# Kernel tuning notes

Hardware: AMD Instinct MI355X
Metric: run time of the kernel (lower is better)

Reference implementation:

```python
import jax, jax.numpy as jnp
import numpy as np

B, S, D, H = 2, 2048, 1024, 16
DK = D // H

def setup_inputs() -> dict:
    key = jax.random.key(0)
    ks = jax.random.split(key, 11)
    scale = 1.0 / np.sqrt(D)
    inp = {
        'query': jax.random.normal(ks[0], (B, S, D), jnp.float32),
        'key':   jax.random.normal(ks[1], (B, S, D), jnp.float32),
        'value': jax.random.normal(ks[2], (B, S, D), jnp.float32),
        'wq': jax.random.normal(ks[3], (D, D), jnp.float32) * scale,
        'bq': jax.random.normal(ks[4], (D,), jnp.float32) * 0.01,
        'wk': jax.random.normal(ks[5], (D, D), jnp.float32) * scale,
        'bk': jax.random.normal(ks[6], (D,), jnp.float32) * 0.01,
        'wv': jax.random.normal(ks[7], (D, D), jnp.float32) * scale,
        'bv': jax.random.normal(ks[8], (D,), jnp.float32) * 0.01,
        'wo': jax.random.normal(ks[9], (D, D), jnp.float32) * scale,
        'bo': jax.random.normal(ks[10], (D,), jnp.float32) * 0.01,
    }
    return inp

def reference(query, key, value, wq, bq, wk, bk, wv, bv, wo, bo):
    nb = query.shape[0]
    # projections: torch nn.Linear computes x @ W^T + b; here weights stored as (in,out)
    def proj(x, w, b):
        return (x @ w + b).reshape(nb, -1, H, DK).transpose(0, 2, 1, 3)  # [B,H,S,dk]
    q = proj(query, wq, bq)
    k = proj(key, wk, bk)
    v = proj(value, wv, bv)
    scores = jnp.einsum('bhqd,bhkd->bhqk', q, k) / jnp.sqrt(jnp.float32(DK))
    p = jax.nn.softmax(scores, axis=-1)  # dropout p=0 (eval)
    x = jnp.einsum('bhqk,bhkd->bhqd', p, v)
    x = x.transpose(0, 2, 1, 3).reshape(nb, -1, H * DK)
    return x @ wo + bo
```

## Files before the change

kernel.cpp:

```cpp
#include <hip/hip_runtime.h>


typedef __attribute__((ext_vector_type(8))) __bf16 bf16x8;
typedef __attribute__((ext_vector_type(4))) __bf16 bf16x4;
typedef __attribute__((ext_vector_type(8))) float f32x8;
typedef __attribute__((ext_vector_type(4))) float f32x4;

#define MFMA16 __builtin_amdgcn_mfma_f32_16x16x32_bf16

union Bf8 { bf16x8 v; __bf16 e[8]; };

__device__ inline f32x4 zero4() { f32x4 z; z[0]=z[1]=z[2]=z[3]=0.f; return z; }

__global__ __launch_bounds__(256) void prep_w(
        const float* __restrict__ w0, const float* __restrict__ w1,
        const float* __restrict__ w2, const float* __restrict__ w3,
        __bf16* __restrict__ wt) {
    const float* src = blockIdx.z == 0 ? w0 : blockIdx.z == 1 ? w1 :
                       blockIdx.z == 2 ? w2 : w3;
    __bf16* dst = wt + (size_t)blockIdx.z * 1048576;
    __shared__ float tile[32][33];
    const int t = threadIdx.x;
    const int tc = t & 31, tr = t >> 5;
    const int r0 = blockIdx.y * 32, c0 = blockIdx.x * 32;
#pragma unroll
    for (int i = 0; i < 4; i++) {
        int r = tr + i * 8;
        tile[r][tc] = src[(size_t)(r0 + r) * 1024 + c0 + tc];
    }
    __syncthreads();
#pragma unroll
    for (int i = 0; i < 4; i++) {
        int r = tr + i * 8;
        dst[(size_t)(c0 + r) * 1024 + r0 + tc] = (__bf16)tile[tc][r];
    }
}

__global__ __launch_bounds__(256) void prep_x(
        const float* __restrict__ x0, const float* __restrict__ x1,
        const float* __restrict__ x2, __bf16* __restrict__ xb) {
    const float* src = blockIdx.y == 0 ? x0 : blockIdx.y == 1 ? x1 : x2;
    __bf16* dst = xb + (size_t)blockIdx.y * 4194304;
    size_t g = ((size_t)blockIdx.x * 256 + threadIdx.x) * 8;
    f32x8 a = *(const f32x8*)&src[g];
    Bf8 tmp;
#pragma unroll
    for (int j = 0; j < 8; j++) tmp.e[j] = (__bf16)a[j];
    *(bf16x8*)&dst[g] = tmp.v;
}

template <int MODE, bool AF32, typename OutT>
__device__ inline void gemm_core(const void* __restrict__ Av,
                                 const __bf16* __restrict__ Bt,
                                 const float* __restrict__ bias,
                                 OutT* __restrict__ out) {
    __shared__ __bf16 As[128 * 72];
    __shared__ __bf16 Bs[128 * 72];
    const int t = threadIdx.x;
    const int wave = t >> 6, lane = t & 63, lm = lane & 15, quad = lane >> 4;
    const int m0 = blockIdx.y * 128, n0 = blockIdx.x * 128;
    const int wm = (wave >> 1) * 64, wn = (wave & 1) * 64;

    f32x4 acc[4][4];
#pragma unroll
    for (int i = 0; i < 4; i++)
#pragma unroll
        for (int j = 0; j < 4; j++) acc[i][j] = zero4();

    for (int k0 = 0; k0 < 1024; k0 += 64) {
#pragma unroll
        for (int i = 0; i < 4; i++) {
            int c = i * 256 + t;
            int row = c >> 3, c8 = c & 7;
            size_t aoff = (size_t)(m0 + row) * 1024 + k0 + c8 * 8;
            if (AF32) {
                f32x8 a = *(const f32x8*)&((const float*)Av)[aoff];
                Bf8 tmp;
#pragma unroll
                for (int j = 0; j < 8; j++) tmp.e[j] = (__bf16)a[j];
                *(bf16x8*)&As[row * 72 + c8 * 8] = tmp.v;
            } else {
                *(bf16x8*)&As[row * 72 + c8 * 8] =
                    *(const bf16x8*)&((const __bf16*)Av)[aoff];
            }
            *(bf16x8*)&Bs[row * 72 + c8 * 8] =
                *(const bf16x8*)&Bt[(size_t)(n0 + row) * 1024 + k0 + c8 * 8];
        }
        __syncthreads();
#pragma unroll
        for (int ks = 0; ks < 2; ks++) {
            bf16x8 af[4], bfr[4];
#pragma unroll
            for (int mt = 0; mt < 4; mt++)
                af[mt] = *(const bf16x8*)&As[(wm + mt * 16 + lm) * 72 + ks * 32 + quad * 8];
#pragma unroll
            for (int nt = 0; nt < 4; nt++)
                bfr[nt] = *(const bf16x8*)&Bs[(wn + nt * 16 + lm) * 72 + ks * 32 + quad * 8];
#pragma unroll
            for (int mt = 0; mt < 4; mt++)
#pragma unroll
                for (int nt = 0; nt < 4; nt++)
                    acc[mt][nt] = MFMA16(af[mt], bfr[nt], acc[mt][nt], 0, 0, 0);
        }
        __syncthreads();
    }

    float bv4[4];
#pragma unroll
    for (int nt = 0; nt < 4; nt++) bv4[nt] = bias[n0 + wn + nt * 16 + lm];

#pragma unroll
    for (int mt = 0; mt < 4; mt++) {
#pragma unroll
        for (int r = 0; r < 4; r++) {
            int row = m0 + wm + mt * 16 + quad * 4 + r;
#pragma unroll
            for (int nt = 0; nt < 4; nt++) {
                int col = n0 + wn + nt * 16 + lm;
                float val = acc[mt][nt][r] + bv4[nt];
                size_t idx;
                if (MODE == 0) {
                    idx = (size_t)row * 1024 + col;
                } else {
                    int b = row >> 11, s = row & 2047, hh = col >> 6, dk = col & 63;
                    if (MODE == 1)
                        idx = (size_t)(b * 16 + hh) * 131072 + (size_t)s * 64 + dk;
                    else
                        idx = (size_t)(b * 16 + hh) * 131072 + (size_t)dk * 2048 + s;
                }
                out[idx] = (OutT)val;
            }
        }
    }
}

template <bool AF32>
__global__ __launch_bounds__(256) void proj_kernel(
        const void* __restrict__ q, const void* __restrict__ k,
        const void* __restrict__ v, const __bf16* __restrict__ WT,
        const float* __restrict__ bq, const float* __restrict__ bk,
        const float* __restrict__ bv,
        __bf16* __restrict__ Q, __bf16* __restrict__ K, __bf16* __restrict__ Vt) {
    int z = blockIdx.z;
    if (z == 0)      gemm_core<1, AF32, __bf16>(q, WT,           bq, Q);
    else if (z == 1) gemm_core<1, AF32, __bf16>(k, WT + 1048576, bk, K);
    else             gemm_core<2, AF32, __bf16>(v, WT + 2097152, bv, Vt);
}

__global__ __launch_bounds__(256) void out_proj_kernel(
        const __bf16* __restrict__ A, const __bf16* __restrict__ Bt,
        const float* __restrict__ bias, float* __restrict__ out) {
    gemm_core<0, false, float>(A, Bt, bias, out);
}

__global__ __launch_bounds__(256, 2) void attn_kernel(
        const __bf16* __restrict__ Q, const __bf16* __restrict__ K,
        const __bf16* __restrict__ Vt, __bf16* __restrict__ O) {
    __shared__ __bf16 Ks[128 * 72];
    __shared__ __bf16 Vs[64 * 136];
    __shared__ __bf16 Ps[4 * 32 * 136];
    const int t = threadIdx.x;
    const int wave = t >> 6, lane = t & 63, lm = lane & 15, quad = lane >> 4;
    const int q0 = blockIdx.x * 128;
    const int bh = blockIdx.y;
    const size_t base = (size_t)bh * 131072;

    bf16x8 bq[2][2];
    {
        int qrow = q0 + wave * 32;
#pragma unroll
        for (int nt = 0; nt < 2; nt++)
#pragma unroll
            for (int ks = 0; ks < 2; ks++)
                bq[nt][ks] = *(const bf16x8*)
                    &Q[base + (size_t)(qrow + nt * 16 + lm) * 64 + ks * 32 + quad * 8];
    }

    float m_run[2], l_run[2];
#pragma unroll
    for (int n = 0; n < 2; n++) { m_run[n] = -1e30f; l_run[n] = 0.f; }
    f32x4 o_acc[4][2];
#pragma unroll
    for (int mt = 0; mt < 4; mt++)
#pragma unroll
        for (int n = 0; n < 2; n++) o_acc[mt][n] = zero4();

    __bf16* Pw = &Ps[wave * 32 * 136];

    for (int kv0 = 0; kv0 < 2048; kv0 += 128) {
#pragma unroll
        for (int i = 0; i < 4; i++) {
            int c = i * 256 + t;
            {
                int row = c >> 3, c8 = c & 7;
                *(bf16x8*)&Ks[row * 72 + c8 * 8] =
                    *(const bf16x8*)&K[base + (size_t)(kv0 + row) * 64 + c8 * 8];
            }
            {
                int row = c >> 4, c16 = c & 15;
                *(bf16x8*)&Vs[row * 136 + c16 * 8] =
                    *(const bf16x8*)&Vt[base + (size_t)row * 2048 + kv0 + c16 * 8];
            }
        }
        __syncthreads();

        f32x4 sc[8][2];
#pragma unroll
        for (int mt = 0; mt < 8; mt++) {
            sc[mt][0] = zero4();
            sc[mt][1] = zero4();
#pragma unroll
            for (int ks = 0; ks < 2; ks++) {
                bf16x8 ak = *(const bf16x8*)&Ks[(mt * 16 + lm) * 72 + ks * 32 + quad * 8];
                sc[mt][0] = MFMA16(ak, bq[0][ks], sc[mt][0], 0, 0, 0);
                sc[mt][1] = MFMA16(ak, bq[1][ks], sc[mt][1], 0, 0, 0);
            }
        }

#pragma unroll
        for (int nt = 0; nt < 2; nt++) {
            float mx = -1e30f;
#pragma unroll
            for (int mt = 0; mt < 8; mt++)
#pragma unroll
                for (int r = 0; r < 4; r++) {
                    sc[mt][nt][r] *= 0.125f;
                    mx = fmaxf(mx, sc[mt][nt][r]);
                }
            mx = fmaxf(mx, __shfl_xor(mx, 16));
            mx = fmaxf(mx, __shfl_xor(mx, 32));
            float mn = fmaxf(m_run[nt], mx);
            float alpha = __expf(m_run[nt] - mn);
            m_run[nt] = mn;
            float su = 0.f;
#pragma unroll
            for (int mt = 0; mt < 8; mt++)
#pragma unroll
                for (int r = 0; r < 4; r++) {
                    float p = __expf(sc[mt][nt][r] - mn);
                    sc[mt][nt][r] = p;
                    su += p;
                }
            su += __shfl_xor(su, 16);
            su += __shfl_xor(su, 32);
            l_run[nt] = l_run[nt] * alpha + su;
#pragma unroll
            for (int mt = 0; mt < 4; mt++)
#pragma unroll
                for (int r = 0; r < 4; r++) o_acc[mt][nt][r] *= alpha;
        }

#pragma unroll
        for (int nt = 0; nt < 2; nt++)
#pragma unroll
            for (int mt = 0; mt < 8; mt++) {
                bf16x4 pk;
#pragma unroll
                for (int r = 0; r < 4; r++) pk[r] = (__bf16)sc[mt][nt][r];
                *(bf16x4*)&Pw[(nt * 16 + lm) * 136 + mt * 16 + quad * 4] = pk;
            }
        __asm__ volatile("" ::: "memory");

#pragma unroll
        for (int ks = 0; ks < 4; ks++) {
            bf16x8 bp[2];
#pragma unroll
            for (int nt = 0; nt < 2; nt++)
                bp[nt] = *(const bf16x8*)&Pw[(nt * 16 + lm) * 136 + ks * 32 + quad * 8];
#pragma unroll
            for (int mt = 0; mt < 4; mt++) {
                bf16x8 av = *(const bf16x8*)&Vs[(mt * 16 + lm) * 136 + ks * 32 + quad * 8];
                o_acc[mt][0] = MFMA16(av, bp[0], o_acc[mt][0], 0, 0, 0);
                o_acc[mt][1] = MFMA16(av, bp[1], o_acc[mt][1], 0, 0, 0);
            }
        }
        __syncthreads();
    }

#pragma unroll
    for (int nt = 0; nt < 2; nt++) {
        float inv = 1.f / l_run[nt];
#pragma unroll
        for (int mt = 0; mt < 4; mt++) {
            bf16x4 pk;
#pragma unroll
            for (int r = 0; r < 4; r++) pk[r] = (__bf16)(o_acc[mt][nt][r] * inv);
            *(bf16x4*)&Pw[(nt * 16 + lm) * 136 + mt * 16 + quad * 4] = pk;
        }
    }
    __asm__ volatile("" ::: "memory");
    {
        const int b = bh >> 4, h = bh & 15;
        int ql = lane >> 1, half = lane & 1;
        int srow = q0 + wave * 32 + ql;
#pragma unroll
        for (int j = 0; j < 4; j++) {
            bf16x8 v = *(const bf16x8*)&Pw[ql * 136 + half * 32 + j * 8];
            *(bf16x8*)&O[(size_t)(b * 2048 + srow) * 1024 + h * 64 + half * 32 + j * 8] = v;
        }
    }
}

extern "C" void kernel_launch(void* const* d_in, const int* in_sizes, int n_in,
                              void* d_out, int out_size, void* d_ws, size_t ws_size,
                              hipStream_t stream) {
    if (ws_size < ((size_t)40 << 20)) return;

    const float* query = (const float*)d_in[0];
    const float* key_  = (const float*)d_in[1];
    const float* value = (const float*)d_in[2];
    const float* wq = (const float*)d_in[3];
    const float* bq = (const float*)d_in[4];
    const float* wk = (const float*)d_in[5];
    const float* bk = (const float*)d_in[6];
    const float* wv = (const float*)d_in[7];
    const float* bv = (const float*)d_in[8];
    const float* wo = (const float*)d_in[9];
    const float* bo = (const float*)d_in[10];
    float* out = (float*)d_out;

    char* ws = (char*)d_ws;
    const bool big = ws_size >= ((size_t)72 << 20);
    __bf16* WT  = (__bf16*)(ws);
    __bf16* Xb  = (__bf16*)(ws + ((size_t)8 << 20));
    size_t o0 = big ? ((size_t)32 << 20) : ((size_t)8 << 20);
    __bf16* Qw  = (__bf16*)(ws + o0);
    __bf16* Kw  = (__bf16*)(ws + o0 + ((size_t)8 << 20));
    __bf16* Vtw = (__bf16*)(ws + o0 + ((size_t)16 << 20));
    __bf16* Ow  = (__bf16*)(ws + o0 + ((size_t)24 << 20));

    prep_w<<<dim3(32, 32, 4), dim3(256), 0, stream>>>(wq, wk, wv, wo, WT);
    if (big) {
        prep_x<<<dim3(2048, 3), dim3(256), 0, stream>>>(query, key_, value, Xb);
        proj_kernel<false><<<dim3(8, 32, 3), dim3(256), 0, stream>>>(
            Xb, Xb + 4194304, Xb + 8388608, WT, bq, bk, bv, Qw, Kw, Vtw);
    } else {
        proj_kernel<true><<<dim3(8, 32, 3), dim3(256), 0, stream>>>(
            query, key_, value, WT, bq, bk, bv, Qw, Kw, Vtw);
    }
    attn_kernel<<<dim3(16, 32), dim3(256), 0, stream>>>(Qw, Kw, Vtw, Ow);
    out_proj_kernel<<<dim3(8, 32), dim3(256), 0, stream>>>(
        Ow, WT + 3 * 1048576, bo, out);
}
```

Measured before the change: 255.0 us.

## Use direct global-to-LDS loads with XOR swizzle, fuse prep kernels, fold softmax scale

Global-to-shared tile staging in the projection GEMMs and the attention K/V loads now uses the async global_load_lds builtin with an XOR-swizzled, unpadded LDS layout in place of register round-trips into padded arrays. The weight and activation conversion kernels are merged into one launch. The 1/sqrt(dk) scale moves into the Q projection epilogue so the attention loop no longer multiplies every score. Workspace layout is reshuffled so the bf16 input buffer is reused for the attention output, which lowers the threshold for the fast path. The risk is that the swizzle indexing must exactly match the per-wave LDS destination ordering of the builtin.

```diff
diff --git a/kernel.cpp b/kernel.cpp
--- a/kernel.cpp
+++ b/kernel.cpp
@@ -12,50 +12,60 @@
 
 __device__ inline f32x4 zero4() { f32x4 z; z[0]=z[1]=z[2]=z[3]=0.f; return z; }
 
-__global__ __launch_bounds__(256) void prep_w(
+__device__ inline void load_lds16(const void* g, void* l) {
+    __builtin_amdgcn_global_load_lds(
+        (const __attribute__((address_space(1))) unsigned int*)g,
+        (__attribute__((address_space(3))) unsigned int*)l, 16, 0, 0);
+}
+
+__global__ __launch_bounds__(256) void prep_all(
         const float* __restrict__ w0, const float* __restrict__ w1,
         const float* __restrict__ w2, const float* __restrict__ w3,
-        __bf16* __restrict__ wt) {
-    const float* src = blockIdx.z == 0 ? w0 : blockIdx.z == 1 ? w1 :
-                       blockIdx.z == 2 ? w2 : w3;
-    __bf16* dst = wt + (size_t)blockIdx.z * 1048576;
-    __shared__ float tile[32][33];
+        const float* __restrict__ x0, const float* __restrict__ x1,
+        const float* __restrict__ x2,
+        __bf16* __restrict__ wt, __bf16* __restrict__ xb) {
+    const int z = blockIdx.z;
     const int t = threadIdx.x;
-    const int tc = t & 31, tr = t >> 5;
-    const int r0 = blockIdx.y * 32, c0 = blockIdx.x * 32;
-#pragma unroll
-    for (int i = 0; i < 4; i++) {
-        int r = tr + i * 8;
-        tile[r][tc] = src[(size_t)(r0 + r) * 1024 + c0 + tc];
-    }
-    __syncthreads();
-#pragma unroll
-    for (int i = 0; i < 4; i++) {
-        int r = tr + i * 8;
-        dst[(size_t)(c0 + r) * 1024 + r0 + tc] = (__bf16)tile[tc][r];
-    }
-}
-
-__global__ __launch_bounds__(256) void prep_x(
-        const float* __restrict__ x0, const float* __restrict__ x1,
-        const float* __restrict__ x2, __bf16* __restrict__ xb) {
-    const float* src = blockIdx.y == 0 ? x0 : blockIdx.y == 1 ? x1 : x2;
-    __bf16* dst = xb + (size_t)blockIdx.y * 4194304;
-    size_t g = ((size_t)blockIdx.x * 256 + threadIdx.x) * 8;
-    f32x8 a = *(const f32x8*)&src[g];
-    Bf8 tmp;
-#pragma unroll
-    for (int j = 0; j < 8; j++) tmp.e[j] = (__bf16)a[j];
-    *(bf16x8*)&dst[g] = tmp.v;
-}
-
-template <int MODE, bool AF32, typename OutT>
-__device__ inline void gemm_core(const void* __restrict__ Av,
-                                 const __bf16* __restrict__ Bt,
-                                 const float* __restrict__ bias,
-                                 OutT* __restrict__ out) {
-    __shared__ __bf16 As[128 * 72];
-    __shared__ __bf16 Bs[128 * 72];
+    if (z < 4) {
+        const float* src = z == 0 ? w0 : z == 1 ? w1 : z == 2 ? w2 : w3;
+        __bf16* dst = wt + (size_t)z * 1048576;
+        __shared__ float tile[32][33];
+        const int tc = t & 31, tr = t >> 5;
+        const int r0 = blockIdx.y * 32, c0 = blockIdx.x * 32;
+#pragma unroll
+        for (int i = 0; i < 4; i++) {
+            int r = tr + i * 8;
+            tile[r][tc] = src[(size_t)(r0 + r) * 1024 + c0 + tc];
+        }
+        __syncthreads();
+#pragma unroll
+        for (int i = 0; i < 4; i++) {
+            int r = tr + i * 8;
+            dst[(size_t)(c0 + r) * 1024 + r0 + tc] = (__bf16)tile[tc][r];
+        }
+    } else {
+        const float* src = z == 4 ? x0 : z == 5 ? x1 : x2;
+        __bf16* dst = xb + (size_t)(z - 4) * 4194304;
+        int bid = blockIdx.y * 32 + blockIdx.x;
+        size_t g = ((size_t)bid * 256 + t) * 16;
+#pragma unroll
+        for (int h = 0; h < 2; h++) {
+            f32x8 a = *(const f32x8*)&src[g + h * 8];
+            Bf8 tmp;
+#pragma unroll
+            for (int j = 0; j < 8; j++) tmp.e[j] = (__bf16)a[j];
+            *(bf16x8*)&dst[g + h * 8] = tmp.v;
+        }
+    }
+}
+
+template <int MODE, typename OutT>
+__device__ inline void gemm_fast_core(const __bf16* __restrict__ A,
+                                      const __bf16* __restrict__ Bt,
+                                      const float* __restrict__ bias,
+                                      OutT* __restrict__ out, float scale) {
+    __shared__ __bf16 As[8192];
+    __shared__ __bf16 Bs[8192];
     const int t = threadIdx.x;
     const int wave = t >> 6, lane = t & 63, lm = lane & 15, quad = lane >> 4;
     const int m0 = blockIdx.y * 128, n0 = blockIdx.x * 128;
@@ -70,21 +80,13 @@
     for (int k0 = 0; k0 < 1024; k0 += 64) {
 #pragma unroll
         for (int i = 0; i < 4; i++) {
-            int c = i * 256 + t;
-            int row = c >> 3, c8 = c & 7;
-            size_t aoff = (size_t)(m0 + row) * 1024 + k0 + c8 * 8;
-            if (AF32) {
-                f32x8 a = *(const f32x8*)&((const float*)Av)[aoff];
-                Bf8 tmp;
-#pragma unroll
-                for (int j = 0; j < 8; j++) tmp.e[j] = (__bf16)a[j];
-                *(bf16x8*)&As[row * 72 + c8 * 8] = tmp.v;
-            } else {
-                *(bf16x8*)&As[row * 72 + c8 * 8] =
-                    *(const bf16x8*)&((const __bf16*)Av)[aoff];
-            }
-            *(bf16x8*)&Bs[row * 72 + c8 * 8] =
-                *(const bf16x8*)&Bt[(size_t)(n0 + row) * 1024 + k0 + c8 * 8];
+            int s = i * 256 + t;
+            int row = s >> 3, cb = (s & 7) ^ (row & 7);
+            size_t goff = (size_t)row * 1024 + k0 + cb * 8;
+            __bf16* lbase = (__bf16*)((size_t)(i * 256 + wave * 64) * 8);
+            load_lds16(&A[(size_t)m0 * 1024 + goff], &As[(size_t)(i * 256 + wave * 64) * 8]);
+            load_lds16(&Bt[(size_t)n0 * 1024 + goff], &Bs[(size_t)(i * 256 + wave * 64) * 8]);
+            (void)lbase;
         }
         __syncthreads();
 #pragma unroll
@@ -92,10 +94,12 @@
             bf16x8 af[4], bfr[4];
 #pragma unroll
             for (int mt = 0; mt < 4; mt++)
-                af[mt] = *(const bf16x8*)&As[(wm + mt * 16 + lm) * 72 + ks * 32 + quad * 8];
+                af[mt] = *(const bf16x8*)&As[(wm + mt * 16 + lm) * 64 +
+                                             (((ks * 4 + quad) ^ (lm & 7)) * 8)];
 #pragma unroll
             for (int nt = 0; nt < 4; nt++)
-                bfr[nt] = *(const bf16x8*)&Bs[(wn + nt * 16 + lm) * 72 + ks * 32 + quad * 8];
+                bfr[nt] = *(const bf16x8*)&Bs[(wn + nt * 16 + lm) * 64 +
+                                              (((ks * 4 + quad) ^ (lm & 7)) * 8)];
 #pragma unroll
             for (int mt = 0; mt < 4; mt++)
 #pragma unroll
@@ -117,7 +121,7 @@
 #pragma unroll
             for (int nt = 0; nt < 4; nt++) {
                 int col = n0 + wn + nt * 16 + lm;
-                float val = acc[mt][nt][r] + bv4[nt];
+                float val = (acc[mt][nt][r] + bv4[nt]) * scale;
                 size_t idx;
                 if (MODE == 0) {
                     idx = (size_t)row * 1024 + col;
@@ -134,30 +138,119 @@
     }
 }
 
-template <bool AF32>
-__global__ __launch_bounds__(256) void proj_kernel(
-        const void* __restrict__ q, const void* __restrict__ k,
-        const void* __restrict__ v, const __bf16* __restrict__ WT,
+__global__ __launch_bounds__(256) void proj_fast(
+        const __bf16* __restrict__ Xb, const __bf16* __restrict__ WT,
         const float* __restrict__ bq, const float* __restrict__ bk,
         const float* __restrict__ bv,
         __bf16* __restrict__ Q, __bf16* __restrict__ K, __bf16* __restrict__ Vt) {
     int z = blockIdx.z;
-    if (z == 0)      gemm_core<1, AF32, __bf16>(q, WT,           bq, Q);
-    else if (z == 1) gemm_core<1, AF32, __bf16>(k, WT + 1048576, bk, K);
-    else             gemm_core<2, AF32, __bf16>(v, WT + 2097152, bv, Vt);
-}
-
-__global__ __launch_bounds__(256) void out_proj_kernel(
+    if (z == 0)
+        gemm_fast_core<1, __bf16>(Xb, WT, bq, Q, 0.125f);
+    else if (z == 1)
+        gemm_fast_core<1, __bf16>(Xb + 4194304, WT + 1048576, bk, K, 1.f);
+    else
+        gemm_fast_core<2, __bf16>(Xb + 8388608, WT + 2097152, bv, Vt, 1.f);
+}
+
+__global__ __launch_bounds__(256) void out_proj_fast(
         const __bf16* __restrict__ A, const __bf16* __restrict__ Bt,
         const float* __restrict__ bias, float* __restrict__ out) {
-    gemm_core<0, false, float>(A, Bt, bias, out);
+    gemm_fast_core<0, float>(A, Bt, bias, out, 1.f);
+}
+
+template <int MODE>
+__device__ inline void gemm_core(const float* __restrict__ A,
+                                 const __bf16* __restrict__ Bt,
+                                 const float* __restrict__ bias,
+                                 __bf16* __restrict__ out, float scale) {
+    __shared__ __bf16 As[128 * 72];
+    __shared__ __bf16 Bs[128 * 72];
+    const int t = threadIdx.x;
+    const int wave = t >> 6, lane = t & 63, lm = lane & 15, quad = lane >> 4;
+    const int m0 = blockIdx.y * 128, n0 = blockIdx.x * 128;
+    const int wm = (wave >> 1) * 64, wn = (wave & 1) * 64;
+
+    f32x4 acc[4][4];
+#pragma unroll
+    for (int i = 0; i < 4; i++)
+#pragma unroll
+        for (int j = 0; j < 4; j++) acc[i][j] = zero4();
+
+    for (int k0 = 0; k0 < 1024; k0 += 64) {
+#pragma unroll
+        for (int i = 0; i < 4; i++) {
+            int c = i * 256 + t;
+            int row = c >> 3, c8 = c & 7;
+            size_t aoff = (size_t)(m0 + row) * 1024 + k0 + c8 * 8;
+            f32x8 a = *(const f32x8*)&A[aoff];
+            Bf8 tmp;
+#pragma unroll
+            for (int j = 0; j < 8; j++) tmp.e[j] = (__bf16)a[j];
+            *(bf16x8*)&As[row * 72 + c8 * 8] = tmp.v;
+            *(bf16x8*)&Bs[row * 72 + c8 * 8] =
+                *(const bf16x8*)&Bt[(size_t)(n0 + row) * 1024 + k0 + c8 * 8];
+        }
+        __syncthreads();
+#pragma unroll
+        for (int ks = 0; ks < 2; ks++) {
+            bf16x8 af[4], bfr[4];
+#pragma unroll
+            for (int mt = 0; mt < 4; mt++)
+                af[mt] = *(const bf16x8*)&As[(wm + mt * 16 + lm) * 72 + ks * 32 + quad * 8];
+#pragma unroll
+            for (int nt = 0; nt < 4; nt++)
+                bfr[nt] = *(const bf16x8*)&Bs[(wn + nt * 16 + lm) * 72 + ks * 32 + quad * 8];
+#pragma unroll
+            for (int mt = 0; mt < 4; mt++)
+#pragma unroll
+                for (int nt = 0; nt < 4; nt++)
+                    acc[mt][nt] = MFMA16(af[mt], bfr[nt], acc[mt][nt], 0, 0, 0);
+        }
+        __syncthreads();
+    }
+
+    float bv4[4];
+#pragma unroll
+    for (int nt = 0; nt < 4; nt++) bv4[nt] = bias[n0 + wn + nt * 16 + lm];
+
+#pragma unroll
+    for (int mt = 0; mt < 4; mt++) {
+#pragma unroll
+        for (int r = 0; r < 4; r++) {
+            int row = m0 + wm + mt * 16 + quad * 4 + r;
+#pragma unroll
+            for (int nt = 0; nt < 4; nt++) {
+                int col = n0 + wn + nt * 16 + lm;
+                float val = (acc[mt][nt][r] + bv4[nt]) * scale;
+                size_t idx;
+                int b = row >> 11, s = row & 2047, hh = col >> 6, dk = col & 63;
+                if (MODE == 1)
+                    idx = (size_t)(b * 16 + hh) * 131072 + (size_t)s * 64 + dk;
+                else
+                    idx = (size_t)(b * 16 + hh) * 131072 + (size_t)dk * 2048 + s;
+                out[idx] = (__bf16)val;
+            }
+        }
+    }
+}
+
+__global__ __launch_bounds__(256) void proj_slow(
+        const float* __restrict__ q, const float* __restrict__ k,
+        const float* __restrict__ v, const __bf16* __restrict__ WT,
+        const float* __restrict__ bq, const float* __restrict__ bk,
+        const float* __restrict__ bv,
+        __bf16* __restrict__ Q, __bf16* __restrict__ K, __bf16* __restrict__ Vt) {
+    int z = blockIdx.z;
+    if (z == 0)      gemm_core<1>(q, WT,           bq, Q,  0.125f);
+    else if (z == 1) gemm_core<1>(k, WT + 1048576, bk, K,  1.f);
+    else             gemm_core<2>(v, WT + 2097152, bv, Vt, 1.f);
 }
 
 __global__ __launch_bounds__(256, 2) void attn_kernel(
         const __bf16* __restrict__ Q, const __bf16* __restrict__ K,
         const __bf16* __restrict__ Vt, __bf16* __restrict__ O) {
-    __shared__ __bf16 Ks[128 * 72];
-    __shared__ __bf16 Vs[64 * 136];
+    __shared__ __bf16 Ks[8192];
+    __shared__ __bf16 Vs[8192];
     __shared__ __bf16 Ps[4 * 32 * 136];
     const int t = threadIdx.x;
     const int wave = t >> 6, lane = t & 63, lm = lane & 15, quad = lane >> 4;
@@ -190,16 +283,16 @@
     for (int kv0 = 0; kv0 < 2048; kv0 += 128) {
 #pragma unroll
         for (int i = 0; i < 4; i++) {
-            int c = i * 256 + t;
+            int s = i * 256 + t;
             {
-                int row = c >> 3, c8 = c & 7;
-                *(bf16x8*)&Ks[row * 72 + c8 * 8] =
-                    *(const bf16x8*)&K[base + (size_t)(kv0 + row) * 64 + c8 * 8];
+                int row = s >> 3, cb = (s & 7) ^ (row & 7);
+                load_lds16(&K[base + (size_t)(kv0 + row) * 64 + cb * 8],
+                           &Ks[(size_t)(i * 256 + wave * 64) * 8]);
             }
             {
-                int row = c >> 4, c16 = c & 15;
-                *(bf16x8*)&Vs[row * 136 + c16 * 8] =
-                    *(const bf16x8*)&Vt[base + (size_t)row * 2048 + kv0 + c16 * 8];
+                int row = s >> 4, cb = (s & 15) ^ (row & 15);
+                load_lds16(&Vt[base + (size_t)row * 2048 + kv0 + cb * 8],
+                           &Vs[(size_t)(i * 256 + wave * 64) * 8]);
             }
         }
         __syncthreads();
@@ -211,7 +304,8 @@
             sc[mt][1] = zero4();
 #pragma unroll
             for (int ks = 0; ks < 2; ks++) {
-                bf16x8 ak = *(const bf16x8*)&Ks[(mt * 16 + lm) * 72 + ks * 32 + quad * 8];
+                bf16x8 ak = *(const bf16x8*)&Ks[(mt * 16 + lm) * 64 +
+                                                (((ks * 4 + quad) ^ (lm & 7)) * 8)];
                 sc[mt][0] = MFMA16(ak, bq[0][ks], sc[mt][0], 0, 0, 0);
                 sc[mt][1] = MFMA16(ak, bq[1][ks], sc[mt][1], 0, 0, 0);
             }
@@ -223,10 +317,7 @@
 #pragma unroll
             for (int mt = 0; mt < 8; mt++)
 #pragma unroll
-                for (int r = 0; r < 4; r++) {
-                    sc[mt][nt][r] *= 0.125f;
-                    mx = fmaxf(mx, sc[mt][nt][r]);
-                }
+                for (int r = 0; r < 4; r++) mx = fmaxf(mx, sc[mt][nt][r]);
             mx = fmaxf(mx, __shfl_xor(mx, 16));
             mx = fmaxf(mx, __shfl_xor(mx, 32));
             float mn = fmaxf(m_run[nt], mx);
@@ -269,7 +360,8 @@
                 bp[nt] = *(const bf16x8*)&Pw[(nt * 16 + lm) * 136 + ks * 32 + quad * 8];
 #pragma unroll
             for (int mt = 0; mt < 4; mt++) {
-                bf16x8 av = *(const bf16x8*)&Vs[(mt * 16 + lm) * 136 + ks * 32 + quad * 8];
+                bf16x8 av = *(const bf16x8*)&Vs[(mt * 16 + lm) * 128 +
+                                                (((ks * 4 + quad) ^ lm) * 8)];
                 o_acc[mt][0] = MFMA16(av, bp[0], o_acc[mt][0], 0, 0, 0);
                 o_acc[mt][1] = MFMA16(av, bp[1], o_acc[mt][1], 0, 0, 0);
             }
@@ -320,25 +412,33 @@
     float* out = (float*)d_out;
 
     char* ws = (char*)d_ws;
-    const bool big = ws_size >= ((size_t)72 << 20);
-    __bf16* WT  = (__bf16*)(ws);
-    __bf16* Xb  = (__bf16*)(ws + ((size_t)8 << 20));
-    size_t o0 = big ? ((size_t)32 << 20) : ((size_t)8 << 20);
-    __bf16* Qw  = (__bf16*)(ws + o0);
-    __bf16* Kw  = (__bf16*)(ws + o0 + ((size_t)8 << 20));
-    __bf16* Vtw = (__bf16*)(ws + o0 + ((size_t)16 << 20));
-    __bf16* Ow  = (__bf16*)(ws + o0 + ((size_t)24 << 20));
-
-    prep_w<<<dim3(32, 32, 4), dim3(256), 0, stream>>>(wq, wk, wv, wo, WT);
+    const bool big = ws_size >= ((size_t)56 << 20);
+    __bf16* WT = (__bf16*)(ws);
+
     if (big) {
-        prep_x<<<dim3(2048, 3), dim3(256), 0, stream>>>(query, key_, value, Xb);
-        proj_kernel<false><<<dim3(8, 32, 3), dim3(256), 0, stream>>>(
-            Xb, Xb + 4194304, Xb + 8388608, WT, bq, bk, bv, Qw, Kw, Vtw);
+        __bf16* Xb  = (__bf16*)(ws + ((size_t)8 << 20));
+        __bf16* Ow  = (__bf16*)(ws + ((size_t)8 << 20));
+        __bf16* Qw  = (__bf16*)(ws + ((size_t)32 << 20));
+        __bf16* Kw  = (__bf16*)(ws + ((size_t)40 << 20));
+        __bf16* Vtw = (__bf16*)(ws + ((size_t)48 << 20));
+        prep_all<<<dim3(32, 32, 7), dim3(256), 0, stream>>>(
+            wq, wk, wv, wo, query, key_, value, WT, Xb);
+        proj_fast<<<dim3(8, 32, 3), dim3(256), 0, stream>>>(
+            Xb, WT, bq, bk, bv, Qw, Kw, Vtw);
+        attn_kernel<<<dim3(16, 32), dim3(256), 0, stream>>>(Qw, Kw, Vtw, Ow);
+        out_proj_fast<<<dim3(8, 32), dim3(256), 0, stream>>>(
+            Ow, WT + 3 * 1048576, bo, out);
     } else {
-        proj_kernel<true><<<dim3(8, 32, 3), dim3(256), 0, stream>>>(
+        __bf16* Qw  = (__bf16*)(ws + ((size_t)8 << 20));
+        __bf16* Kw  = (__bf16*)(ws + ((size_t)16 << 20));
+        __bf16* Vtw = (__bf16*)(ws + ((size_t)24 << 20));
+        __bf16* Ow  = (__bf16*)(ws + ((size_t)32 << 20));
+        prep_all<<<dim3(32, 32, 4), dim3(256), 0, stream>>>(
+            wq, wk, wv, wo, query, key_, value, WT, (__bf16*)nullptr);
+        proj_slow<<<dim3(8, 32, 3), dim3(256), 0, stream>>>(
             query, key_, value, WT, bq, bk, bv, Qw, Kw, Vtw);
-    }
-    attn_kernel<<<dim3(16, 32), dim3(256), 0, stream>>>(Qw, Kw, Vtw, Ow);
-    out_proj_kernel<<<dim3(8, 32), dim3(256), 0, stream>>>(
-        Ow, WT + 3 * 1048576, bo, out);
-}
+        attn_kernel<<<dim3(16, 32), dim3(256), 0, stream>>>(Qw, Kw, Vtw, Ow);
+        out_proj_fast<<<dim3(8, 32), dim3(256), 0, stream>>>(
+            Ow, WT + 3 * 1048576, bo, out);
+    }
+}
```

Measured after the change: 244.2 us. 1.04x faster.
